# Kernel optimization log

Measured on AMD Instinct MI355X. Metric: run time of the kernel, lower is better.

## Reference

```python
import jax, jax.numpy as jnp
import numpy as np

CAPACITY = 2  # module init arg


def setup_inputs() -> dict:
    B, S, D, E, I = 4, 4096, 1024, 8, 4096
    key = jax.random.key(0)
    k0, k1, k2, k3, k4 = jax.random.split(key, 5)
    x = jax.random.normal(k0, (B, S, D), dtype=jnp.float32)
    # nn.init.normal_(gate_weight, std=0.006)
    gate_w = jax.random.normal(k1, (E, D), dtype=jnp.float32) * 0.006
    w_gate = jax.random.normal(k2, (E, I, D), dtype=jnp.float32) * (1.0 / np.sqrt(D))
    w_up = jax.random.normal(k3, (E, I, D), dtype=jnp.float32) * (1.0 / np.sqrt(D))
    w_down = jax.random.normal(k4, (E, D, I), dtype=jnp.float32) * (1.0 / np.sqrt(I))
    return {"x": x, "gate_w": gate_w, "w_gate": w_gate, "w_up": w_up, "w_down": w_down}


def reference(x, gate_w, w_gate, w_up, w_down):
    # Expert-choice MoE. The torch code materializes a one-hot dispatch tensor
    # (B,E,C,S) and contracts it with x / x_e; mathematically that is exactly an
    # indexed gather (dispatch) and scatter-add (combine), which we do directly.
    B, S, D = x.shape
    E = gate_w.shape[0]
    k = (S // E) * CAPACITY  # capacity per expert

    logits = jnp.einsum('bsd,ed->bse', x, gate_w)
    affinity = jax.nn.softmax(logits, axis=-1)              # softmax over experts
    affinity = jnp.transpose(affinity, (0, 2, 1))           # (B,E,S)
    gating, idx = jax.lax.top_k(affinity, k)                # each expert picks k tokens; (B,E,k)

    bidx = jnp.arange(B)[:, None, None]                     # (B,1,1) broadcast vs (B,E,k)
    x_in = x[bidx, idx]                                     # gather: (B,E,k,D)

    # per-expert gated SiLU MLP: down(silu(gate(x)) * up(x))
    h = jax.nn.silu(jnp.einsum('bekd,eid->beki', x_in, w_gate)) \
        * jnp.einsum('bekd,eid->beki', x_in, w_up)          # (B,E,k,I)
    x_e = jnp.einsum('beki,edi->bekd', h, w_down)           # (B,E,k,D)

    # combine: scatter-add gated expert outputs back to token positions
    out = jnp.zeros_like(x).at[bidx, idx].add(gating[..., None] * x_e)
    return out
```

## Files before the change

kernel.cpp:

```cpp
#include <hip/hip_runtime.h>
#include <hip/hip_bf16.h>


#define B_ 4
#define S_ 4096
#define D_ 1024
#define E_ 8
#define I_ 4096
#define KCAP 1024
#define NGROUPS 32

typedef __bf16 bf16x8 __attribute__((ext_vector_type(8)));
typedef float floatx4 __attribute__((ext_vector_type(4)));

#define GLD16(gptr, lptr)                                          \
  __builtin_amdgcn_global_load_lds(                                \
      (const __attribute__((address_space(1))) void*)(gptr),       \
      (__attribute__((address_space(3))) void*)(lptr), 16, 0, 0)

__device__ __forceinline__ float bf2f(unsigned short h) {
  union { unsigned int u; float f; } v; v.u = ((unsigned int)h) << 16; return v.f;
}
__device__ __forceinline__ unsigned short f2bf(float f) {
  union { float f; unsigned int u; } v; v.f = f;
  unsigned int r = (v.u + 0x7fffu + ((v.u >> 16) & 1u)) >> 16;
  return (unsigned short)r;
}

__global__ __launch_bounds__(256) void probe_dtype_k(const unsigned short* __restrict__ xr,
                                                     int* __restrict__ flag) {
  __shared__ unsigned int cnt;
  if (threadIdx.x == 0) cnt = 0;
  __syncthreads();
  unsigned int local = 0;
  for (int j = 0; j < 16; ++j) {
    int k = threadIdx.x * 16 + j;
    unsigned short u = xr[2 * k];
    unsigned int expf = (u >> 7) & 0xFF;
    if (expf >= 0x90 && expf != 0xFF) local++;
    if (expf == 0xFF) local++;
  }
  atomicAdd(&cnt, local);
  __syncthreads();
  if (threadIdx.x == 0) *flag = (cnt > 256u) ? 1 : 0;
}

__global__ __launch_bounds__(256) void conv_in_k(const void* __restrict__ src,
                                                 unsigned short* __restrict__ dst,
                                                 const int* __restrict__ flag) {
  const int isf32 = *flag;
  size_t i = ((size_t)blockIdx.x * 256 + threadIdx.x) * 8;
  if (isf32) {
    const float* s = (const float*)src;
    float4 a = *(const float4*)(s + i);
    float4 b = *(const float4*)(s + i + 4);
    ushort4 o0, o1;
    o0.x = f2bf(a.x); o0.y = f2bf(a.y); o0.z = f2bf(a.z); o0.w = f2bf(a.w);
    o1.x = f2bf(b.x); o1.y = f2bf(b.y); o1.z = f2bf(b.z); o1.w = f2bf(b.w);
    *(ushort4*)(dst + i) = o0;
    *(ushort4*)(dst + i + 4) = o1;
  } else {
    const uint4* s = (const uint4*)src;
    *(uint4*)(dst + i) = s[i / 8];
  }
}

__global__ __launch_bounds__(256) void gate_softmax_k(
    const void* __restrict__ xr, const void* __restrict__ gwr,
    const int* __restrict__ flag, double* __restrict__ aff) {
  const int isf32 = *flag;
  const int wave = threadIdx.x >> 6, lane = threadIdx.x & 63;
  const int token = blockIdx.x * 4 + wave;
  double acc[E_];
#pragma unroll
  for (int e2 = 0; e2 < E_; ++e2) acc[e2] = 0.0;
  for (int j = 0; j < 16; ++j) {
    int k = lane + 64 * j;
    double xv, wv[E_];
    if (isf32) {
      xv = (double)((const float*)xr)[(size_t)token * D_ + k];
#pragma unroll
      for (int e2 = 0; e2 < E_; ++e2) wv[e2] = (double)((const float*)gwr)[e2 * D_ + k];
    } else {
      xv = (double)bf2f(((const unsigned short*)xr)[(size_t)token * D_ + k]);
#pragma unroll
      for (int e2 = 0; e2 < E_; ++e2) wv[e2] = (double)bf2f(((const unsigned short*)gwr)[e2 * D_ + k]);
    }
#pragma unroll
    for (int e2 = 0; e2 < E_; ++e2) acc[e2] += xv * wv[e2];
  }
#pragma unroll
  for (int e2 = 0; e2 < E_; ++e2) {
#pragma unroll
    for (int off = 1; off < 64; off <<= 1) acc[e2] += __shfl_xor(acc[e2], off);
  }
  if (lane < E_) {
    double mx = acc[0];
#pragma unroll
    for (int e2 = 1; e2 < E_; ++e2) mx = acc[e2] > mx ? acc[e2] : mx;
    double ssum = 0.0;
#pragma unroll
    for (int e2 = 0; e2 < E_; ++e2) ssum += exp(acc[e2] - mx);
    double p = exp(acc[lane] - mx) / ssum;
    int b = token >> 12, s = token & (S_ - 1);
    aff[((size_t)b * E_ + lane) * S_ + s] = p;
  }
}

__global__ __launch_bounds__(256) void topk_sel_k(
    const double* __restrict__ aff, int* __restrict__ sel_idx, float* __restrict__ sel_gate) {
  __shared__ unsigned long long keys[4096];
  __shared__ unsigned int hist[256];
  __shared__ unsigned int bcast[3];
  const int g = blockIdx.x, t = threadIdx.x;
  const int e = g >> 2, b = g & 3;
  const double* ap = aff + ((size_t)b * E_ + e) * S_;
  for (int j = 0; j < 16; ++j) {
    int i = t + 256 * j;
    keys[i] = __double_as_longlong(ap[i]);
  }
  __syncthreads();
  unsigned long long prefix = 0ull;
  int remaining = KCAP;
  for (int p = 7; p >= 0; --p) {
    hist[t] = 0;
    __syncthreads();
    unsigned long long mask_hi = (p == 7) ? 0ull : (~0ull << ((p + 1) * 8));
    for (int j = 0; j < 16; ++j) {
      unsigned long long key = keys[t + 256 * j];
      if ((key & mask_hi) == prefix)
        atomicAdd(&hist[(unsigned)(key >> (p * 8)) & 255u], 1u);
    }
    __syncthreads();
    if (t == 0) {
      unsigned cum = 0; int bsel = 0;
      for (int v = 255; v >= 0; --v) {
        unsigned cc = hist[v];
        if (cum + cc >= (unsigned)remaining) { bsel = v; break; }
        cum += cc;
      }
      bcast[0] = (unsigned)bsel; bcast[1] = cum;
    }
    __syncthreads();
    prefix |= ((unsigned long long)bcast[0]) << (p * 8);
    remaining -= (int)bcast[1];
    __syncthreads();
  }
  if (t == 0) bcast[2] = 0;
  __syncthreads();
  const unsigned long long T = prefix;
  for (int j = 0; j < 16; ++j) {
    int i = t + 256 * j;
    unsigned long long key = keys[i];
    if (key > T) {
      unsigned pos = atomicAdd(&bcast[2], 1u);
      sel_idx[g * KCAP + pos] = i;
      sel_gate[g * KCAP + pos] = (float)__longlong_as_double(key);
    }
  }
  __syncthreads();
  for (int j = 0; j < 16; ++j) {
    int i = t + 256 * j;
    unsigned long long key = keys[i];
    if (key == T) {
      unsigned pos = atomicAdd(&bcast[2], 1u);
      if (pos < KCAP) {
        sel_idx[g * KCAP + pos] = i;
        sel_gate[g * KCAP + pos] = (float)__longlong_as_double(key);
      }
    }
  }
}

__global__ __launch_bounds__(256) void moe_gemm1(
    const unsigned short* __restrict__ x, const unsigned short* __restrict__ w_gate,
    const unsigned short* __restrict__ w_up, const int* __restrict__ sel_idx,
    unsigned short* __restrict__ hbuf, int chunk_start) {
  __shared__ __align__(16) unsigned short sA[128 * 32];
  __shared__ __align__(16) unsigned short sG[64 * 32];
  __shared__ __align__(16) unsigned short sU[64 * 32];
  const int gc = blockIdx.z;
  const int g = chunk_start + gc;
  const int e = g >> 2, b = g & 3;
  const int m0 = blockIdx.x * 128, n0 = blockIdx.y * 64;
  const int t = threadIdx.x;
  const int r = t >> 2, c = (t & 3) * 8;

  const int tok0 = sel_idx[g * KCAP + m0 + r] & (S_ - 1);
  const int tok1 = sel_idx[g * KCAP + m0 + 64 + r] & (S_ - 1);
  const unsigned short* gA0 = x + ((size_t)b * S_ + tok0) * D_ + c;
  const unsigned short* gA1 = x + ((size_t)b * S_ + tok1) * D_ + c;
  const unsigned short* gG = w_gate + ((size_t)e * I_ + n0 + r) * D_ + c;
  const unsigned short* gU = w_up + ((size_t)e * I_ + n0 + r) * D_ + c;

  const int wave = t >> 6, lane = t & 63;
  const int wm = wave >> 1, wn = wave & 1;
  const int row16 = lane & 15, quad = lane >> 4;

  unsigned short* lA0 = sA + wave * 512;
  unsigned short* lA1 = sA + 2048 + wave * 512;
  unsigned short* lG = sG + wave * 512;
  unsigned short* lU = sU + wave * 512;

  floatx4 accg[4][2], accu[4][2];
#pragma unroll
  for (int ms = 0; ms < 4; ++ms)
#pragma unroll
    for (int ns = 0; ns < 2; ++ns) {
      accg[ms][ns] = (floatx4){0.f, 0.f, 0.f, 0.f};
      accu[ms][ns] = (floatx4){0.f, 0.f, 0.f, 0.f};
    }

  for (int k0 = 0; k0 < D_; k0 += 32) {
    __syncthreads();
    GLD16(gA0 + k0, lA0);
    GLD16(gA1 + k0, lA1);
    GLD16(gG + k0, lG);
    GLD16(gU + k0, lU);
    __syncthreads();
    bf16x8 a[4], bg[2], bu[2];
#pragma unroll
    for (int ms = 0; ms < 4; ++ms)
      a[ms] = *(const bf16x8*)(sA + (wm * 64 + ms * 16 + row16) * 32 + quad * 8);
#pragma unroll
    for (int ns = 0; ns < 2; ++ns) {
      bg[ns] = *(const bf16x8*)(sG + (wn * 32 + ns * 16 + row16) * 32 + quad * 8);
      bu[ns] = *(const bf16x8*)(sU + (wn * 32 + ns * 16 + row16) * 32 + quad * 8);
    }
#pragma unroll
    for (int ms = 0; ms < 4; ++ms)
#pragma unroll
      for (int ns = 0; ns < 2; ++ns) {
        accg[ms][ns] = __builtin_amdgcn_mfma_f32_16x16x32_bf16(a[ms], bg[ns], accg[ms][ns], 0, 0, 0);
        accu[ms][ns] = __builtin_amdgcn_mfma_f32_16x16x32_bf16(a[ms], bu[ns], accu[ms][ns], 0, 0, 0);
      }
  }
  unsigned short* hb = hbuf + (size_t)gc * ((size_t)KCAP * I_);
#pragma unroll
  for (int ms = 0; ms < 4; ++ms)
#pragma unroll
    for (int ns = 0; ns < 2; ++ns)
#pragma unroll
      for (int r4 = 0; r4 < 4; ++r4) {
        int m = m0 + wm * 64 + ms * 16 + quad * 4 + r4;
        int n = n0 + wn * 32 + ns * 16 + row16;
        float gv = accg[ms][ns][r4], uv = accu[ms][ns][r4];
        float hv = gv / (1.f + __expf(-gv)) * uv;
        hb[(size_t)m * I_ + n] = f2bf(hv);
      }
}

__global__ __launch_bounds__(256) void moe_gemm2(
    const unsigned short* __restrict__ hbuf, const unsigned short* __restrict__ w_down,
    const int* __restrict__ sel_idx, const float* __restrict__ sel_gate,
    float* __restrict__ acc_out, int chunk_start) {
  __shared__ __align__(16) unsigned short sA[128 * 32];
  __shared__ __align__(16) unsigned short sB[128 * 32];
  __shared__ int stok[128];
  __shared__ float sgt[128];
  const int gc = blockIdx.z;
  const int g = chunk_start + gc;
  const int e = g >> 2, b = g & 3;
  const int m0 = blockIdx.x * 128, n0 = blockIdx.y * 128;
  const int t = threadIdx.x;
  const int r = t >> 2, c = (t & 3) * 8;
  if (t < 128) {
    stok[t] = sel_idx[g * KCAP + m0 + t] & (S_ - 1);
    sgt[t] = sel_gate[g * KCAP + m0 + t];
  }
  const unsigned short* gA0 = hbuf + (size_t)gc * ((size_t)KCAP * I_) + (size_t)(m0 + r) * I_ + c;
  const unsigned short* gA1 = gA0 + (size_t)64 * I_;
  const unsigned short* gB0 = w_down + ((size_t)e * D_ + n0 + r) * I_ + c;
  const unsigned short* gB1 = gB0 + (size_t)64 * I_;
  const int wave = t >> 6, lane = t & 63;
  const int wm = wave >> 1, wn = wave & 1;
  const int row16 = lane & 15, quad = lane >> 4;

  unsigned short* lA0 = sA + wave * 512;
  unsigned short* lA1 = sA + 2048 + wave * 512;
  unsigned short* lB0 = sB + wave * 512;
  unsigned short* lB1 = sB + 2048 + wave * 512;

  floatx4 accf[4][4];
#pragma unroll
  for (int ms = 0; ms < 4; ++ms)
#pragma unroll
    for (int ns = 0; ns < 4; ++ns) accf[ms][ns] = (floatx4){0.f, 0.f, 0.f, 0.f};

  for (int k0 = 0; k0 < I_; k0 += 32) {
    __syncthreads();
    GLD16(gA0 + k0, lA0);
    GLD16(gA1 + k0, lA1);
    GLD16(gB0 + k0, lB0);
    GLD16(gB1 + k0, lB1);
    __syncthreads();
    bf16x8 a[4], bb[4];
#pragma unroll
    for (int i = 0; i < 4; ++i) {
      a[i] = *(const bf16x8*)(sA + (wm * 64 + i * 16 + row16) * 32 + quad * 8);
      bb[i] = *(const bf16x8*)(sB + (wn * 64 + i * 16 + row16) * 32 + quad * 8);
    }
#pragma unroll
    for (int ms = 0; ms < 4; ++ms)
#pragma unroll
      for (int ns = 0; ns < 4; ++ns)
        accf[ms][ns] = __builtin_amdgcn_mfma_f32_16x16x32_bf16(a[ms], bb[ns], accf[ms][ns], 0, 0, 0);
  }
#pragma unroll
  for (int ms = 0; ms < 4; ++ms)
#pragma unroll
    for (int r4 = 0; r4 < 4; ++r4) {
      int mloc = wm * 64 + ms * 16 + quad * 4 + r4;
      int tok = stok[mloc];
      float gt = sgt[mloc];
      float* basep = acc_out + ((size_t)b * S_ + tok) * D_ + n0 + wn * 64 + row16;
#pragma unroll
      for (int ns = 0; ns < 4; ++ns) unsafeAtomicAdd(basep + ns * 16, accf[ms][ns][r4] * gt);
    }
}

__global__ __launch_bounds__(256) void conv_out_k(const float* __restrict__ acc,
                                                  void* __restrict__ out,
                                                  const int* __restrict__ flag) {
  const int isf32 = *flag;
  size_t i = ((size_t)blockIdx.x * 256 + threadIdx.x) * 4;
  float4 v = *(const float4*)(acc + i);
  if (isf32) {
    *(float4*)((float*)out + i) = v;
  } else {
    ushort4 o;
    o.x = f2bf(v.x); o.y = f2bf(v.y); o.z = f2bf(v.z); o.w = f2bf(v.w);
    *(ushort4*)((unsigned short*)out + i) = o;
  }
}

extern "C" void kernel_launch(void* const* d_in, const int* in_sizes, int n_in,
                              void* d_out, int out_size, void* d_ws, size_t ws_size,
                              hipStream_t stream) {
  const void* x_raw = d_in[0];
  const void* gate_w_raw = d_in[1];
  const void* w_gate_raw = d_in[2];
  const void* w_up_raw = d_in[3];
  const void* w_down_raw = d_in[4];

  char* ws = (char*)d_ws;
  size_t off = 0;
  auto alloc = [&](size_t bytes) { char* p = ws + off; off += (bytes + 255) & ~(size_t)255; return p; };
  float* acc = (float*)alloc((size_t)B_ * S_ * D_ * 4);
  double* aff = (double*)alloc((size_t)B_ * E_ * S_ * 8);
  int* sel_idx = (int*)alloc((size_t)NGROUPS * KCAP * 4);
  float* sel_gate = (float*)alloc((size_t)NGROUPS * KCAP * 4);
  int* flag = (int*)alloc(256);
  unsigned short* xb = (unsigned short*)alloc((size_t)B_ * S_ * D_ * 2);
  unsigned short* wgb = (unsigned short*)alloc((size_t)E_ * I_ * D_ * 2);
  unsigned short* wub = (unsigned short*)alloc((size_t)E_ * I_ * D_ * 2);
  unsigned short* wdb = (unsigned short*)alloc((size_t)E_ * D_ * I_ * 2);
  const size_t fixedBytes = off;
  const size_t hPerGroup = (size_t)KCAP * I_ * 2;
  int gch = 32;
  while (gch > 1 && fixedBytes + (size_t)gch * hPerGroup > ws_size) gch >>= 1;
  unsigned short* hbuf = (unsigned short*)(ws + fixedBytes);

  hipMemsetAsync(acc, 0, (size_t)B_ * S_ * D_ * 4, stream);
  hipMemsetAsync(sel_idx, 0, (size_t)NGROUPS * KCAP * 8, stream);

  probe_dtype_k<<<dim3(1), dim3(256), 0, stream>>>((const unsigned short*)x_raw, flag);
  conv_in_k<<<dim3((int)((size_t)B_ * S_ * D_ / 2048)), dim3(256), 0, stream>>>(x_raw, xb, flag);
  conv_in_k<<<dim3((int)((size_t)E_ * I_ * D_ / 2048)), dim3(256), 0, stream>>>(w_gate_raw, wgb, flag);
  conv_in_k<<<dim3((int)((size_t)E_ * I_ * D_ / 2048)), dim3(256), 0, stream>>>(w_up_raw, wub, flag);
  conv_in_k<<<dim3((int)((size_t)E_ * D_ * I_ / 2048)), dim3(256), 0, stream>>>(w_down_raw, wdb, flag);

  gate_softmax_k<<<dim3(B_ * S_ / 4), dim3(256), 0, stream>>>(x_raw, gate_w_raw, flag, aff);
  topk_sel_k<<<dim3(NGROUPS), dim3(256), 0, stream>>>(aff, sel_idx, sel_gate);
  for (int c0 = 0; c0 < NGROUPS; c0 += gch) {
    int gcur = (NGROUPS - c0) < gch ? (NGROUPS - c0) : gch;
    moe_gemm1<<<dim3(KCAP / 128, I_ / 64, gcur), dim3(256), 0, stream>>>(
        xb, wgb, wub, sel_idx, hbuf, c0);
    moe_gemm2<<<dim3(KCAP / 128, D_ / 128, gcur), dim3(256), 0, stream>>>(
        hbuf, wdb, sel_idx, sel_gate, acc, c0);
  }
  conv_out_k<<<dim3((int)((size_t)B_ * S_ * D_ / 4 / 256)), dim3(256), 0, stream>>>(acc, d_out, flag);
}
```

Measured before the change: 2.046 ms.

## Double-buffer LDS tiles in both MoE GEMM kernels to overlap loads with MFMA

Both expert GEMM kernels now use two LDS buffers per operand. The next K-slice is issued via global_load_lds while MFMAs run on the current slice, with one barrier per slice instead of two. This is meant to hide global-to-LDS latency behind compute. It doubles LDS use per block, which may reduce occupancy, and relies on the barrier making the async LDS loads visible before they are read.

```diff
diff --git a/kernel.cpp b/kernel.cpp
--- a/kernel.cpp
+++ b/kernel.cpp
@@ -172,13 +172,47 @@
   }
 }
 
+__device__ __forceinline__ void stage1(const unsigned short* gA0, const unsigned short* gA1,
+                                       const unsigned short* gG, const unsigned short* gU,
+                                       unsigned short* SA, unsigned short* SG,
+                                       unsigned short* SU, int wave, int k0) {
+  GLD16(gA0 + k0, SA + wave * 512);
+  GLD16(gA1 + k0, SA + 2048 + wave * 512);
+  GLD16(gG + k0, SG + wave * 512);
+  GLD16(gU + k0, SU + wave * 512);
+}
+
+__device__ __forceinline__ void comp1(const unsigned short* SA, const unsigned short* SG,
+                                      const unsigned short* SU, int wm, int wn, int row16,
+                                      int quad, floatx4 (&accg)[4][2], floatx4 (&accu)[4][2]) {
+  bf16x8 a[4], bg[2], bu[2];
+#pragma unroll
+  for (int ms = 0; ms < 4; ++ms)
+    a[ms] = *(const bf16x8*)(SA + (wm * 64 + ms * 16 + row16) * 32 + quad * 8);
+#pragma unroll
+  for (int ns = 0; ns < 2; ++ns) {
+    bg[ns] = *(const bf16x8*)(SG + (wn * 32 + ns * 16 + row16) * 32 + quad * 8);
+    bu[ns] = *(const bf16x8*)(SU + (wn * 32 + ns * 16 + row16) * 32 + quad * 8);
+  }
+#pragma unroll
+  for (int ms = 0; ms < 4; ++ms)
+#pragma unroll
+    for (int ns = 0; ns < 2; ++ns) {
+      accg[ms][ns] = __builtin_amdgcn_mfma_f32_16x16x32_bf16(a[ms], bg[ns], accg[ms][ns], 0, 0, 0);
+      accu[ms][ns] = __builtin_amdgcn_mfma_f32_16x16x32_bf16(a[ms], bu[ns], accu[ms][ns], 0, 0, 0);
+    }
+}
+
 __global__ __launch_bounds__(256) void moe_gemm1(
     const unsigned short* __restrict__ x, const unsigned short* __restrict__ w_gate,
     const unsigned short* __restrict__ w_up, const int* __restrict__ sel_idx,
     unsigned short* __restrict__ hbuf, int chunk_start) {
-  __shared__ __align__(16) unsigned short sA[128 * 32];
-  __shared__ __align__(16) unsigned short sG[64 * 32];
-  __shared__ __align__(16) unsigned short sU[64 * 32];
+  __shared__ __align__(16) unsigned short sA0[128 * 32];
+  __shared__ __align__(16) unsigned short sA1[128 * 32];
+  __shared__ __align__(16) unsigned short sG0[64 * 32];
+  __shared__ __align__(16) unsigned short sG1[64 * 32];
+  __shared__ __align__(16) unsigned short sU0[64 * 32];
+  __shared__ __align__(16) unsigned short sU1[64 * 32];
   const int gc = blockIdx.z;
   const int g = chunk_start + gc;
   const int e = g >> 2, b = g & 3;
@@ -197,11 +231,6 @@
   const int wm = wave >> 1, wn = wave & 1;
   const int row16 = lane & 15, quad = lane >> 4;
 
-  unsigned short* lA0 = sA + wave * 512;
-  unsigned short* lA1 = sA + 2048 + wave * 512;
-  unsigned short* lG = sG + wave * 512;
-  unsigned short* lU = sU + wave * 512;
-
   floatx4 accg[4][2], accu[4][2];
 #pragma unroll
   for (int ms = 0; ms < 4; ++ms)
@@ -211,30 +240,18 @@
       accu[ms][ns] = (floatx4){0.f, 0.f, 0.f, 0.f};
     }
 
-  for (int k0 = 0; k0 < D_; k0 += 32) {
-    __syncthreads();
-    GLD16(gA0 + k0, lA0);
-    GLD16(gA1 + k0, lA1);
-    GLD16(gG + k0, lG);
-    GLD16(gU + k0, lU);
-    __syncthreads();
-    bf16x8 a[4], bg[2], bu[2];
-#pragma unroll
-    for (int ms = 0; ms < 4; ++ms)
-      a[ms] = *(const bf16x8*)(sA + (wm * 64 + ms * 16 + row16) * 32 + quad * 8);
-#pragma unroll
-    for (int ns = 0; ns < 2; ++ns) {
-      bg[ns] = *(const bf16x8*)(sG + (wn * 32 + ns * 16 + row16) * 32 + quad * 8);
-      bu[ns] = *(const bf16x8*)(sU + (wn * 32 + ns * 16 + row16) * 32 + quad * 8);
-    }
-#pragma unroll
-    for (int ms = 0; ms < 4; ++ms)
-#pragma unroll
-      for (int ns = 0; ns < 2; ++ns) {
-        accg[ms][ns] = __builtin_amdgcn_mfma_f32_16x16x32_bf16(a[ms], bg[ns], accg[ms][ns], 0, 0, 0);
-        accu[ms][ns] = __builtin_amdgcn_mfma_f32_16x16x32_bf16(a[ms], bu[ns], accu[ms][ns], 0, 0, 0);
-      }
-  }
+  stage1(gA0, gA1, gG, gU, sA0, sG0, sU0, wave, 0);
+  __syncthreads();
+
+  for (int k0 = 0; k0 < D_; k0 += 64) {
+    stage1(gA0, gA1, gG, gU, sA1, sG1, sU1, wave, k0 + 32);
+    comp1(sA0, sG0, sU0, wm, wn, row16, quad, accg, accu);
+    __syncthreads();
+    if (k0 + 64 < D_) stage1(gA0, gA1, gG, gU, sA0, sG0, sU0, wave, k0 + 64);
+    comp1(sA1, sG1, sU1, wm, wn, row16, quad, accg, accu);
+    __syncthreads();
+  }
+
   unsigned short* hb = hbuf + (size_t)gc * ((size_t)KCAP * I_);
 #pragma unroll
   for (int ms = 0; ms < 4; ++ms)
@@ -250,12 +267,39 @@
       }
 }
 
+__device__ __forceinline__ void stage2(const unsigned short* gA0, const unsigned short* gA1,
+                                       const unsigned short* gB0, const unsigned short* gB1,
+                                       unsigned short* SA, unsigned short* SB, int wave, int k0) {
+  GLD16(gA0 + k0, SA + wave * 512);
+  GLD16(gA1 + k0, SA + 2048 + wave * 512);
+  GLD16(gB0 + k0, SB + wave * 512);
+  GLD16(gB1 + k0, SB + 2048 + wave * 512);
+}
+
+__device__ __forceinline__ void comp2(const unsigned short* SA, const unsigned short* SB,
+                                      int wm, int wn, int row16, int quad,
+                                      floatx4 (&accf)[4][4]) {
+  bf16x8 a[4], bb[4];
+#pragma unroll
+  for (int i = 0; i < 4; ++i) {
+    a[i] = *(const bf16x8*)(SA + (wm * 64 + i * 16 + row16) * 32 + quad * 8);
+    bb[i] = *(const bf16x8*)(SB + (wn * 64 + i * 16 + row16) * 32 + quad * 8);
+  }
+#pragma unroll
+  for (int ms = 0; ms < 4; ++ms)
+#pragma unroll
+    for (int ns = 0; ns < 4; ++ns)
+      accf[ms][ns] = __builtin_amdgcn_mfma_f32_16x16x32_bf16(a[ms], bb[ns], accf[ms][ns], 0, 0, 0);
+}
+
 __global__ __launch_bounds__(256) void moe_gemm2(
     const unsigned short* __restrict__ hbuf, const unsigned short* __restrict__ w_down,
     const int* __restrict__ sel_idx, const float* __restrict__ sel_gate,
     float* __restrict__ acc_out, int chunk_start) {
-  __shared__ __align__(16) unsigned short sA[128 * 32];
-  __shared__ __align__(16) unsigned short sB[128 * 32];
+  __shared__ __align__(16) unsigned short sA0[128 * 32];
+  __shared__ __align__(16) unsigned short sA1[128 * 32];
+  __shared__ __align__(16) unsigned short sB0[128 * 32];
+  __shared__ __align__(16) unsigned short sB1[128 * 32];
   __shared__ int stok[128];
   __shared__ float sgt[128];
   const int gc = blockIdx.z;
@@ -276,36 +320,24 @@
   const int wm = wave >> 1, wn = wave & 1;
   const int row16 = lane & 15, quad = lane >> 4;
 
-  unsigned short* lA0 = sA + wave * 512;
-  unsigned short* lA1 = sA + 2048 + wave * 512;
-  unsigned short* lB0 = sB + wave * 512;
-  unsigned short* lB1 = sB + 2048 + wave * 512;
-
   floatx4 accf[4][4];
 #pragma unroll
   for (int ms = 0; ms < 4; ++ms)
 #pragma unroll
     for (int ns = 0; ns < 4; ++ns) accf[ms][ns] = (floatx4){0.f, 0.f, 0.f, 0.f};
 
-  for (int k0 = 0; k0 < I_; k0 += 32) {
-    __syncthreads();
-    GLD16(gA0 + k0, lA0);
-    GLD16(gA1 + k0, lA1);
-    GLD16(gB0 + k0, lB0);
-    GLD16(gB1 + k0, lB1);
-    __syncthreads();
-    bf16x8 a[4], bb[4];
-#pragma unroll
-    for (int i = 0; i < 4; ++i) {
-      a[i] = *(const bf16x8*)(sA + (wm * 64 + i * 16 + row16) * 32 + quad * 8);
-      bb[i] = *(const bf16x8*)(sB + (wn * 64 + i * 16 + row16) * 32 + quad * 8);
-    }
-#pragma unroll
-    for (int ms = 0; ms < 4; ++ms)
-#pragma unroll
-      for (int ns = 0; ns < 4; ++ns)
-        accf[ms][ns] = __builtin_amdgcn_mfma_f32_16x16x32_bf16(a[ms], bb[ns], accf[ms][ns], 0, 0, 0);
-  }
+  stage2(gA0, gA1, gB0, gB1, sA0, sB0, wave, 0);
+  __syncthreads();
+
+  for (int k0 = 0; k0 < I_; k0 += 64) {
+    stage2(gA0, gA1, gB0, gB1, sA1, sB1, wave, k0 + 32);
+    comp2(sA0, sB0, wm, wn, row16, quad, accf);
+    __syncthreads();
+    if (k0 + 64 < I_) stage2(gA0, gA1, gB0, gB1, sA0, sB0, wave, k0 + 64);
+    comp2(sA1, sB1, wm, wn, row16, quad, accf);
+    __syncthreads();
+  }
+
 #pragma unroll
   for (int ms = 0; ms < 4; ++ms)
 #pragma unroll
```

Result: faster. 1.915 ms (-6.4%).

## Pipeline MoE GEMMs with 4-stage async LDS ring and larger tiles

Applied to the files above, without the earlier changes.

Both expert GEMM kernels move from single-buffered 128x64/128x128 tiles with two full barriers per k-step to 512-thread blocks with 256x128/256x256 tiles. Global-to-LDS loads run through a 4-slot ring with three stages in flight, gated by vmcnt waits and a raw barrier. MFMA blocks run at raised wave priority, and gemm1 remaps block indices to group tiles that share weights. The aim is to hide load latency and raise operand reuse per LDS byte, at the cost of high register pressure (accumulators for 8x2x2 or 8x4 fragments) and fewer blocks per launch.

```diff
diff --git a/kernel.cpp b/kernel.cpp
--- a/kernel.cpp
+++ b/kernel.cpp
@@ -17,6 +17,10 @@
   __builtin_amdgcn_global_load_lds(                                \
       (const __attribute__((address_space(1))) void*)(gptr),       \
       (__attribute__((address_space(3))) void*)(lptr), 16, 0, 0)
+
+#define WAITV(N) asm volatile("s_waitcnt vmcnt(" #N ")" ::: "memory")
+#define RAW_BAR() __builtin_amdgcn_s_barrier()
+#define CFENCE() asm volatile("" ::: "memory")
 
 __device__ __forceinline__ float bf2f(unsigned short h) {
   union { unsigned int u; float f; } v; v.u = ((unsigned int)h) << 16; return v.f;
@@ -172,150 +176,178 @@
   }
 }
 
-__global__ __launch_bounds__(256) void moe_gemm1(
+__global__ __launch_bounds__(512, 2) void moe_gemm1(
     const unsigned short* __restrict__ x, const unsigned short* __restrict__ w_gate,
     const unsigned short* __restrict__ w_up, const int* __restrict__ sel_idx,
     unsigned short* __restrict__ hbuf, int chunk_start) {
-  __shared__ __align__(16) unsigned short sA[128 * 32];
-  __shared__ __align__(16) unsigned short sG[64 * 32];
-  __shared__ __align__(16) unsigned short sU[64 * 32];
+  __shared__ __align__(16) unsigned short lds[4 * 16384];
   const int gc = blockIdx.z;
   const int g = chunk_start + gc;
   const int e = g >> 2, b = g & 3;
-  const int m0 = blockIdx.x * 128, n0 = blockIdx.y * 64;
+  const int lid = blockIdx.x;
+  const int swz = (lid & 7) * 16 + (lid >> 3);
+  const int m0 = (swz & 3) * 256, n0 = (swz >> 2) * 128;
   const int t = threadIdx.x;
-  const int r = t >> 2, c = (t & 3) * 8;
-
-  const int tok0 = sel_idx[g * KCAP + m0 + r] & (S_ - 1);
-  const int tok1 = sel_idx[g * KCAP + m0 + 64 + r] & (S_ - 1);
-  const unsigned short* gA0 = x + ((size_t)b * S_ + tok0) * D_ + c;
-  const unsigned short* gA1 = x + ((size_t)b * S_ + tok1) * D_ + c;
-  const unsigned short* gG = w_gate + ((size_t)e * I_ + n0 + r) * D_ + c;
-  const unsigned short* gU = w_up + ((size_t)e * I_ + n0 + r) * D_ + c;
-
   const int wave = t >> 6, lane = t & 63;
-  const int wm = wave >> 1, wn = wave & 1;
+  const int wm = wave >> 2, wn = wave & 3;
   const int row16 = lane & 15, quad = lane >> 4;
 
-  unsigned short* lA0 = sA + wave * 512;
-  unsigned short* lA1 = sA + 2048 + wave * 512;
-  unsigned short* lG = sG + wave * 512;
-  unsigned short* lU = sU + wave * 512;
-
-  floatx4 accg[4][2], accu[4][2];
-#pragma unroll
-  for (int ms = 0; ms < 4; ++ms)
-#pragma unroll
-    for (int ns = 0; ns < 2; ++ns) {
-      accg[ms][ns] = (floatx4){0.f, 0.f, 0.f, 0.f};
-      accu[ms][ns] = (floatx4){0.f, 0.f, 0.f, 0.f};
-    }
-
-  for (int k0 = 0; k0 < D_; k0 += 32) {
-    __syncthreads();
-    GLD16(gA0 + k0, lA0);
-    GLD16(gA1 + k0, lA1);
-    GLD16(gG + k0, lG);
-    GLD16(gU + k0, lU);
-    __syncthreads();
-    bf16x8 a[4], bg[2], bu[2];
-#pragma unroll
-    for (int ms = 0; ms < 4; ++ms)
-      a[ms] = *(const bf16x8*)(sA + (wm * 64 + ms * 16 + row16) * 32 + quad * 8);
-#pragma unroll
-    for (int ns = 0; ns < 2; ++ns) {
-      bg[ns] = *(const bf16x8*)(sG + (wn * 32 + ns * 16 + row16) * 32 + quad * 8);
-      bu[ns] = *(const bf16x8*)(sU + (wn * 32 + ns * 16 + row16) * 32 + quad * 8);
-    }
-#pragma unroll
-    for (int ms = 0; ms < 4; ++ms)
-#pragma unroll
-      for (int ns = 0; ns < 2; ++ns) {
-        accg[ms][ns] = __builtin_amdgcn_mfma_f32_16x16x32_bf16(a[ms], bg[ns], accg[ms][ns], 0, 0, 0);
-        accu[ms][ns] = __builtin_amdgcn_mfma_f32_16x16x32_bf16(a[ms], bu[ns], accu[ms][ns], 0, 0, 0);
+  const int atok = sel_idx[g * KCAP + m0 + (t & 255)] & (S_ - 1);
+  const unsigned short* gA = x + ((size_t)b * S_ + atok) * D_ + (t >> 8) * 8;
+  const unsigned short* gG = w_gate + ((size_t)e * I_ + n0 + (t & 127)) * D_ + (t >> 7) * 8;
+  const unsigned short* gU = w_up + ((size_t)e * I_ + n0 + (t & 127)) * D_ + (t >> 7) * 8;
+
+  floatx4 accg[8][2], accu[8][2];
+#pragma unroll
+  for (int m = 0; m < 8; ++m)
+#pragma unroll
+    for (int n = 0; n < 2; ++n) {
+      accg[m][n] = (floatx4){0.f, 0.f, 0.f, 0.f};
+      accu[m][n] = (floatx4){0.f, 0.f, 0.f, 0.f};
+    }
+
+#define STG1(KT, SL) do {                                   \
+    unsigned short* sb_ = lds + (SL) * 16384;               \
+    const int k0_ = (KT) * 32;                              \
+    GLD16(gA + k0_,      sb_ + wave * 512);                 \
+    GLD16(gA + k0_ + 16, sb_ + 4096 + wave * 512);          \
+    GLD16(gG + k0_,      sb_ + 8192 + wave * 512);          \
+    GLD16(gU + k0_,      sb_ + 12288 + wave * 512);         \
+  } while (0)
+
+#define COMP1(SL) do {                                                              \
+    const unsigned short* sb_ = lds + (SL) * 16384;                                 \
+    bf16x8 af[8], gf[2], uf[2];                                                     \
+    _Pragma("unroll")                                                               \
+    for (int m = 0; m < 8; ++m)                                                     \
+      af[m] = *(const bf16x8*)(sb_ + (quad * 256 + wm * 128 + m * 16 + row16) * 8); \
+    _Pragma("unroll")                                                               \
+    for (int n = 0; n < 2; ++n) {                                                   \
+      gf[n] = *(const bf16x8*)(sb_ + 8192 + (quad * 128 + wn * 32 + n * 16 + row16) * 8);  \
+      uf[n] = *(const bf16x8*)(sb_ + 12288 + (quad * 128 + wn * 32 + n * 16 + row16) * 8); \
+    }                                                                               \
+    __builtin_amdgcn_s_setprio(1);                                                  \
+    _Pragma("unroll")                                                               \
+    for (int m = 0; m < 8; ++m)                                                     \
+      _Pragma("unroll")                                                             \
+      for (int n = 0; n < 2; ++n) {                                                 \
+        accg[m][n] = __builtin_amdgcn_mfma_f32_16x16x32_bf16(af[m], gf[n], accg[m][n], 0, 0, 0); \
+        accu[m][n] = __builtin_amdgcn_mfma_f32_16x16x32_bf16(af[m], uf[n], accu[m][n], 0, 0, 0); \
+      }                                                                             \
+    __builtin_amdgcn_s_setprio(0);                                                  \
+  } while (0)
+
+  STG1(0, 0); CFENCE(); STG1(1, 1); CFENCE(); STG1(2, 2);
+#pragma unroll 4
+  for (int kt = 0; kt < 28; ++kt) {
+    WAITV(8); RAW_BAR();
+    STG1(kt + 3, (kt + 3) & 3);
+    COMP1(kt & 3);
+  }
+  { WAITV(8); RAW_BAR(); STG1(31, 3); COMP1(0); }
+  { WAITV(8); RAW_BAR(); COMP1(1); }
+  { WAITV(4); RAW_BAR(); COMP1(2); }
+  { WAITV(0); RAW_BAR(); COMP1(3); }
+#undef STG1
+#undef COMP1
+
+  unsigned short* hb = hbuf + (size_t)gc * ((size_t)KCAP * I_);
+#pragma unroll
+  for (int m = 0; m < 8; ++m)
+#pragma unroll
+    for (int n = 0; n < 2; ++n)
+#pragma unroll
+      for (int r4 = 0; r4 < 4; ++r4) {
+        int mm = m0 + wm * 128 + m * 16 + quad * 4 + r4;
+        int nn = n0 + wn * 32 + n * 16 + row16;
+        float gv = accg[m][n][r4], uv = accu[m][n][r4];
+        float hv = gv / (1.f + __expf(-gv)) * uv;
+        hb[(size_t)mm * I_ + nn] = f2bf(hv);
       }
-  }
-  unsigned short* hb = hbuf + (size_t)gc * ((size_t)KCAP * I_);
-#pragma unroll
-  for (int ms = 0; ms < 4; ++ms)
-#pragma unroll
-    for (int ns = 0; ns < 2; ++ns)
-#pragma unroll
-      for (int r4 = 0; r4 < 4; ++r4) {
-        int m = m0 + wm * 64 + ms * 16 + quad * 4 + r4;
-        int n = n0 + wn * 32 + ns * 16 + row16;
-        float gv = accg[ms][ns][r4], uv = accu[ms][ns][r4];
-        float hv = gv / (1.f + __expf(-gv)) * uv;
-        hb[(size_t)m * I_ + n] = f2bf(hv);
-      }
-}
-
-__global__ __launch_bounds__(256) void moe_gemm2(
+}
+
+__global__ __launch_bounds__(512, 2) void moe_gemm2(
     const unsigned short* __restrict__ hbuf, const unsigned short* __restrict__ w_down,
     const int* __restrict__ sel_idx, const float* __restrict__ sel_gate,
     float* __restrict__ acc_out, int chunk_start) {
-  __shared__ __align__(16) unsigned short sA[128 * 32];
-  __shared__ __align__(16) unsigned short sB[128 * 32];
-  __shared__ int stok[128];
-  __shared__ float sgt[128];
+  __shared__ __align__(16) unsigned short lds[4 * 16384];
+  __shared__ int stok[256];
+  __shared__ float sgt[256];
   const int gc = blockIdx.z;
   const int g = chunk_start + gc;
   const int e = g >> 2, b = g & 3;
-  const int m0 = blockIdx.x * 128, n0 = blockIdx.y * 128;
+  const int m0 = (blockIdx.x & 3) * 256, n0 = (blockIdx.x >> 2) * 256;
   const int t = threadIdx.x;
-  const int r = t >> 2, c = (t & 3) * 8;
-  if (t < 128) {
+  const int wave = t >> 6, lane = t & 63;
+  const int wm = wave >> 2, wn = wave & 3;
+  const int row16 = lane & 15, quad = lane >> 4;
+
+  if (t < 256) {
     stok[t] = sel_idx[g * KCAP + m0 + t] & (S_ - 1);
     sgt[t] = sel_gate[g * KCAP + m0 + t];
   }
-  const unsigned short* gA0 = hbuf + (size_t)gc * ((size_t)KCAP * I_) + (size_t)(m0 + r) * I_ + c;
-  const unsigned short* gA1 = gA0 + (size_t)64 * I_;
-  const unsigned short* gB0 = w_down + ((size_t)e * D_ + n0 + r) * I_ + c;
-  const unsigned short* gB1 = gB0 + (size_t)64 * I_;
-  const int wave = t >> 6, lane = t & 63;
-  const int wm = wave >> 1, wn = wave & 1;
-  const int row16 = lane & 15, quad = lane >> 4;
-
-  unsigned short* lA0 = sA + wave * 512;
-  unsigned short* lA1 = sA + 2048 + wave * 512;
-  unsigned short* lB0 = sB + wave * 512;
-  unsigned short* lB1 = sB + 2048 + wave * 512;
-
-  floatx4 accf[4][4];
-#pragma unroll
-  for (int ms = 0; ms < 4; ++ms)
-#pragma unroll
-    for (int ns = 0; ns < 4; ++ns) accf[ms][ns] = (floatx4){0.f, 0.f, 0.f, 0.f};
-
-  for (int k0 = 0; k0 < I_; k0 += 32) {
-    __syncthreads();
-    GLD16(gA0 + k0, lA0);
-    GLD16(gA1 + k0, lA1);
-    GLD16(gB0 + k0, lB0);
-    GLD16(gB1 + k0, lB1);
-    __syncthreads();
-    bf16x8 a[4], bb[4];
-#pragma unroll
-    for (int i = 0; i < 4; ++i) {
-      a[i] = *(const bf16x8*)(sA + (wm * 64 + i * 16 + row16) * 32 + quad * 8);
-      bb[i] = *(const bf16x8*)(sB + (wn * 64 + i * 16 + row16) * 32 + quad * 8);
-    }
-#pragma unroll
-    for (int ms = 0; ms < 4; ++ms)
-#pragma unroll
-      for (int ns = 0; ns < 4; ++ns)
-        accf[ms][ns] = __builtin_amdgcn_mfma_f32_16x16x32_bf16(a[ms], bb[ns], accf[ms][ns], 0, 0, 0);
-  }
-#pragma unroll
-  for (int ms = 0; ms < 4; ++ms)
+
+  const unsigned short* gA = hbuf + (size_t)gc * ((size_t)KCAP * I_) +
+                             (size_t)(m0 + (t & 255)) * I_ + (t >> 8) * 8;
+  const unsigned short* gB = w_down + ((size_t)e * D_ + n0 + (t & 255)) * I_ + (t >> 8) * 8;
+
+  floatx4 accf[8][4];
+#pragma unroll
+  for (int m = 0; m < 8; ++m)
+#pragma unroll
+    for (int n = 0; n < 4; ++n) accf[m][n] = (floatx4){0.f, 0.f, 0.f, 0.f};
+
+#define STG2(KT, SL) do {                                   \
+    unsigned short* sb_ = lds + (SL) * 16384;               \
+    const int k0_ = (KT) * 32;                              \
+    GLD16(gA + k0_,      sb_ + wave * 512);                 \
+    GLD16(gA + k0_ + 16, sb_ + 4096 + wave * 512);          \
+    GLD16(gB + k0_,      sb_ + 8192 + wave * 512);          \
+    GLD16(gB + k0_ + 16, sb_ + 12288 + wave * 512);         \
+  } while (0)
+
+#define COMP2(SL) do {                                                              \
+    const unsigned short* sb_ = lds + (SL) * 16384;                                 \
+    bf16x8 af[8], bf[4];                                                            \
+    _Pragma("unroll")                                                               \
+    for (int m = 0; m < 8; ++m)                                                     \
+      af[m] = *(const bf16x8*)(sb_ + (quad * 256 + wm * 128 + m * 16 + row16) * 8); \
+    _Pragma("unroll")                                                               \
+    for (int n = 0; n < 4; ++n)                                                     \
+      bf[n] = *(const bf16x8*)(sb_ + 8192 + (quad * 256 + wn * 64 + n * 16 + row16) * 8); \
+    __builtin_amdgcn_s_setprio(1);                                                  \
+    _Pragma("unroll")                                                               \
+    for (int m = 0; m < 8; ++m)                                                     \
+      _Pragma("unroll")                                                             \
+      for (int n = 0; n < 4; ++n)                                                   \
+        accf[m][n] = __builtin_amdgcn_mfma_f32_16x16x32_bf16(af[m], bf[n], accf[m][n], 0, 0, 0); \
+    __builtin_amdgcn_s_setprio(0);                                                  \
+  } while (0)
+
+  STG2(0, 0); CFENCE(); STG2(1, 1); CFENCE(); STG2(2, 2);
+#pragma unroll 4
+  for (int kt = 0; kt < 124; ++kt) {
+    WAITV(8); RAW_BAR();
+    STG2(kt + 3, (kt + 3) & 3);
+    COMP2(kt & 3);
+  }
+  { WAITV(8); RAW_BAR(); STG2(127, 3); COMP2(0); }
+  { WAITV(8); RAW_BAR(); COMP2(1); }
+  { WAITV(4); RAW_BAR(); COMP2(2); }
+  { WAITV(0); RAW_BAR(); COMP2(3); }
+#undef STG2
+#undef COMP2
+
+#pragma unroll
+  for (int m = 0; m < 8; ++m)
 #pragma unroll
     for (int r4 = 0; r4 < 4; ++r4) {
-      int mloc = wm * 64 + ms * 16 + quad * 4 + r4;
+      int mloc = wm * 128 + m * 16 + quad * 4 + r4;
       int tok = stok[mloc];
       float gt = sgt[mloc];
       float* basep = acc_out + ((size_t)b * S_ + tok) * D_ + n0 + wn * 64 + row16;
 #pragma unroll
-      for (int ns = 0; ns < 4; ++ns) unsafeAtomicAdd(basep + ns * 16, accf[ms][ns][r4] * gt);
+      for (int n = 0; n < 4; ++n) unsafeAtomicAdd(basep + n * 16, accf[m][n][r4] * gt);
     }
 }
 
@@ -374,9 +406,9 @@
   topk_sel_k<<<dim3(NGROUPS), dim3(256), 0, stream>>>(aff, sel_idx, sel_gate);
   for (int c0 = 0; c0 < NGROUPS; c0 += gch) {
     int gcur = (NGROUPS - c0) < gch ? (NGROUPS - c0) : gch;
-    moe_gemm1<<<dim3(KCAP / 128, I_ / 64, gcur), dim3(256), 0, stream>>>(
+    moe_gemm1<<<dim3(128, 1, gcur), dim3(512), 0, stream>>>(
         xb, wgb, wub, sel_idx, hbuf, c0);
-    moe_gemm2<<<dim3(KCAP / 128, D_ / 128, gcur), dim3(256), 0, stream>>>(
+    moe_gemm2<<<dim3(16, 1, gcur), dim3(512), 0, stream>>>(
         hbuf, wdb, sel_idx, sel_gate, acc, c0);
   }
   conv_out_k<<<dim3((int)((size_t)B_ * S_ * D_ / 4 / 256)), dim3(256), 0, stream>>>(acc, d_out, flag);
```

After: 1.951 ms. 1.05x faster.
